# Kernel tuning notes

Measured on AMD Instinct MI355X. Metric: run time of the kernel, lower is better.

The kernel has to match this reference:

```python
import jax, jax.numpy as jnp
import numpy as np

HEADS = 8
DIM = 512
DH = DIM // HEADS          # 64
M = DIM // 2               # 256 landmarks
PINV_ITERS = 6
KER = 33                   # residual depthwise conv kernel size
EPS_LN = 1e-5


def setup_inputs() -> dict:
    key = jax.random.key(0)
    ks = jax.random.split(key, 5)
    b, n, d = 4, 8192, DIM
    inner = HEADS * DH
    x = jax.random.normal(ks[0], (b, n, d), jnp.float32)
    gamma = jnp.ones((d,), jnp.float32)
    beta = jnp.zeros((d,), jnp.float32)
    w_qkv = jax.random.normal(ks[1], (d, inner * 3), jnp.float32) * (d ** -0.5)
    res_kernel = jax.random.normal(ks[2], (HEADS, 1, KER, 1), jnp.float32) * 0.1  # depthwise (groups=heads)
    w_out = jax.random.normal(ks[3], (inner, d), jnp.float32) * (inner ** -0.5)
    b_out = jnp.zeros((d,), jnp.float32)
    return dict(x=x, gamma=gamma, beta=beta, w_qkv=w_qkv,
                res_kernel=res_kernel, w_out=w_out, b_out=b_out)


def _moore_penrose_pinv(x, iters=PINV_ITERS):
    # iterative Moore-Penrose pseudo-inverse (Razavi et al.), matches lucidrains impl
    I = jnp.eye(x.shape[-1], dtype=x.dtype)
    denom = jnp.max(jnp.sum(jnp.abs(x), axis=-1)) * jnp.max(jnp.sum(jnp.abs(x), axis=-2))
    z = jnp.swapaxes(x, -1, -2) / denom
    for _ in range(iters):
        xz = x @ z
        z = 0.25 * z @ (13.0 * I - xz @ (15.0 * I - xz @ (7.0 * I - xz)))
    return z


def _forward(x, gamma, beta, w_qkv, res_kernel, w_out, b_out):
    b, n, d = x.shape
    # pre-norm (LayerNorm)
    mu = jnp.mean(x, axis=-1, keepdims=True)
    var = jnp.var(x, axis=-1, keepdims=True)
    normed = (x - mu) / jnp.sqrt(var + EPS_LN) * gamma + beta
    # left-pad so sequence divisible by num_landmarks (static, 0 here)
    pad = (-n) % M
    xp = jnp.pad(normed, ((0, 0), (pad, 0), (0, 0)))
    N = n + pad
    qkv = xp @ w_qkv                                    # [b,N,3*h*dh]
    q, k, v = jnp.split(qkv, 3, axis=-1)
    to_heads = lambda t: t.reshape(b, N, HEADS, DH).transpose(0, 2, 1, 3)  # [b,h,N,dh]
    q = to_heads(q) * (DH ** -0.5)
    k = to_heads(k)
    v = to_heads(v)
    l = N // M
    q_l = q.reshape(b, HEADS, M, l, DH).mean(axis=3)    # [b,h,m,dh] landmarks
    k_l = k.reshape(b, HEADS, M, l, DH).mean(axis=3)
    attn1 = jax.nn.softmax(jnp.einsum('bhnd,bhmd->bhnm', q, k_l), axis=-1)   # [b,h,N,m]
    attn2 = jax.nn.softmax(jnp.einsum('bhmd,bhld->bhml', q_l, k_l), axis=-1) # [b,h,m,m]
    attn3 = jax.nn.softmax(jnp.einsum('bhmd,bhnd->bhmn', q_l, k), axis=-1)   # [b,h,m,N]
    out = attn1 @ (_moore_penrose_pinv(attn2) @ (attn3 @ v))                 # [b,h,N,dh]
    # depthwise conv residual over v (channels = heads)
    conv = jax.lax.conv_general_dilated(
        v, res_kernel, window_strides=(1, 1),
        padding=((KER // 2, KER // 2), (0, 0)),
        feature_group_count=HEADS,
        dimension_numbers=('NCHW', 'OIHW', 'NCHW'))
    out = out + conv
    out = out.transpose(0, 2, 1, 3).reshape(b, N, HEADS * DH)
    out = out @ w_out + b_out                           # to_out (dropout = identity at eval)
    out = out[:, -n:]                                   # drop left padding
    return x + out                                      # TransLayer residual


def reference(x, gamma, beta, w_qkv, res_kernel, w_out, b_out):
    return _forward(x, gamma, beta, w_qkv, res_kernel, w_out, b_out)
```

## Files before the change

### kernel.cpp

```cpp
#include <hip/hip_runtime.h>
#include <hip/hip_bf16.h>

#define B_ 4
#define N_ 8192
#define D_ 512
#define H_ 8
#define DH_ 64
#define M_ 256
#define LCH 32
#define KER_ 33
#define NSPLIT 16
#define CS (N_/NSPLIT)

typedef __hip_bfloat16 bf16;
typedef __attribute__((ext_vector_type(8))) short short8;
typedef __attribute__((ext_vector_type(4))) float f32x4;

__device__ __forceinline__ float bf2f(bf16 h){ return __bfloat162float(h); }
__device__ __forceinline__ bf16 f2bf(float f){ return __float2bfloat16(f); }
__device__ __forceinline__ f32x4 mfma16(short8 a, short8 b, f32x4 c){
  return __builtin_amdgcn_mfma_f32_16x16x32_bf16(a, b, c, 0, 0, 0);
}

__global__ __launch_bounds__(256) void k_layernorm(const float* __restrict__ x,
    const float* __restrict__ gamma, const float* __restrict__ beta,
    bf16* __restrict__ xn){
  int row = blockIdx.x;
  const float* xr = x + (size_t)row * D_;
  bf16* o = xn + (size_t)row * D_;
  int t = threadIdx.x;
  float v0 = xr[t], v1 = xr[t+256];
  float s = v0+v1, ss = v0*v0 + v1*v1;
  __shared__ float sh[8];
  for (int off=32; off; off>>=1){ s += __shfl_xor(s,off); ss += __shfl_xor(ss,off); }
  int lane = t&63, wid = t>>6;
  if (lane==0){ sh[wid] = s; sh[wid+4] = ss; }
  __syncthreads();
  float S  = sh[0]+sh[1]+sh[2]+sh[3];
  float SS = sh[4]+sh[5]+sh[6]+sh[7];
  float mu = S*(1.f/D_);
  float var = SS*(1.f/D_) - mu*mu;
  float rs = rsqrtf(var + 1e-5f);
  o[t]     = f2bf((v0-mu)*rs*gamma[t]     + beta[t]);
  o[t+256] = f2bf((v1-mu)*rs*gamma[t+256] + beta[t+256]);
}

__global__ __launch_bounds__(256) void k_wt(const float* __restrict__ W, bf16* __restrict__ WT,
    int R, int C){
  int c0 = blockIdx.x*64, r0 = blockIdx.y*64;
  __shared__ float tile[64][65];
  int t = threadIdx.x;
  for (int i=t;i<4096;i+=256){ int r=i>>6, c=i&63; tile[r][c] = W[(size_t)(r0+r)*C + c0+c]; }
  __syncthreads();
  for (int i=t;i<512;i+=256){
    int c=i>>3, rg=i&7;
    short8 o;
    #pragma unroll
    for (int j=0;j<8;j++) ((bf16*)&o)[j] = f2bf(tile[rg*8+j][c]);
    *(short8*)&WT[(size_t)(c0+c)*R + r0 + rg*8] = o;
  }
}

__global__ __launch_bounds__(256, 2) void k_mm_qkv4(const bf16* __restrict__ A, const bf16* __restrict__ WT,
    bf16* __restrict__ qbuf, bf16* __restrict__ kbuf, bf16* __restrict__ vbuf,
    bf16* __restrict__ qlb, bf16* __restrict__ klb){
  __shared__ __align__(16) bf16 smem[3*128*72];
  bf16 (*As)[72]  = (bf16(*)[72])smem;
  bf16 (*Bs0)[72] = (bf16(*)[72])(smem + 128*72);
  bf16 (*Bs1)[72] = (bf16(*)[72])(smem + 2*128*72);
  bf16 (*ebuf)[136] = (bf16(*)[136])smem;
  int t = threadIdx.x;
  int w = t>>6, lane = t&63, qd = lane>>4, n = lane&15;
  int wm = w>>1, wn = w&1;
  int r0 = blockIdx.y*128, c0 = blockIdx.x*256;
  f32x4 acc[2][4][4];
  #pragma unroll
  for (int cb=0;cb<2;cb++)
    #pragma unroll
    for (int i=0;i<4;i++)
      #pragma unroll
      for (int j=0;j<4;j++) acc[cb][i][j] = (f32x4){0.f,0.f,0.f,0.f};
  int srow = t>>3, skc = t&7;
  for (int k0=0; k0<512; k0+=64){
    #pragma unroll
    for (int ch=0; ch<4; ch++){
      int m = ch*32 + srow;
      *(short8*)&As[m][skc*8]  = *(const short8*)&A [(size_t)(r0+m)*512 + k0 + skc*8];
      *(short8*)&Bs0[m][skc*8] = *(const short8*)&WT[(size_t)(c0+m)*512 + k0 + skc*8];
      *(short8*)&Bs1[m][skc*8] = *(const short8*)&WT[(size_t)(c0+128+m)*512 + k0 + skc*8];
    }
    __syncthreads();
    #pragma unroll
    for (int ksub=0; ksub<2; ksub++){
      short8 af[4];
      #pragma unroll
      for (int i=0;i<4;i++) af[i] = *(const short8*)&As[wm*64+i*16+n][ksub*32+qd*8];
      #pragma unroll
      for (int cb=0; cb<2; cb++){
        bf16 (*Bsc)[72] = cb ? Bs1 : Bs0;
        short8 bfr[4];
        #pragma unroll
        for (int j=0;j<4;j++) bfr[j] = *(const short8*)&Bsc[wn*64+j*16+n][ksub*32+qd*8];
        #pragma unroll
        for (int i=0;i<4;i++)
          #pragma unroll
          for (int j=0;j<4;j++) acc[cb][i][j] = mfma16(af[i], bfr[j], acc[cb][i][j]);
      }
    }
    __syncthreads();
  }
  int part = c0 >> 9;
  bf16* dst = (part==0)? qbuf : (part==1)? kbuf : vbuf;
  float scale = (part==0)? 0.125f : 1.f;
  #pragma unroll
  for (int cb=0; cb<2; cb++){
    __syncthreads();
    #pragma unroll
    for (int i=0;i<4;i++)
      #pragma unroll
      for (int j=0;j<4;j++)
        #pragma unroll
        for (int rg=0; rg<4; rg++)
          ebuf[wm*64+i*16+qd*4+rg][wn*64+j*16+n] = f2bf(acc[cb][i][j][rg]*scale);
    __syncthreads();
    #pragma unroll
    for (int rep=0; rep<8; rep++){
      int unit = rep*256 + t;
      int row = unit >> 4, ch = unit & 15;
      int col = c0 + cb*128 + ch*8;
      int cc = col & 511, h = cc>>6, dh = cc&63;
      int r = r0 + row, b = r>>13, nn = r&8191;
      *(short8*)&dst[(((size_t)(b*H_+h))*N_ + nn)*DH_ + dh] = *(const short8*)&ebuf[row][ch*8];
    }
    if (part < 2){
      bf16* lt = (part==0) ? qlb : klb;
      #pragma unroll
      for (int rep=0; rep<2; rep++){
        int oi = rep*256 + t;
        int chunk = oi >> 7, col = oi & 127;
        float sum = 0.f;
        #pragma unroll
        for (int rr=0; rr<32; rr++) sum += bf2f(ebuf[chunk*32+rr][col]);
        int r = r0 + chunk*32;
        int b = r >> 13, m = (r & 8191) >> 5;
        int cc = (c0 + cb*128 + col) & 511;
        int h = cc >> 6, dh = cc & 63;
        lt[(((size_t)(b*H_+h))*M_ + m)*DH_ + dh] = f2bf(sum * (1.f/LCH));
      }
    }
  }
}

__global__ __launch_bounds__(256) void k_transp_v(const bf16* __restrict__ v, bf16* __restrict__ vT){
  int bh = blockIdx.y, n0 = blockIdx.x*64;
  __shared__ bf16 tile[64][72];
  const bf16* vb = v + (size_t)bh*N_*DH_;
  int t = threadIdx.x;
  for (int i=t; i<512; i+=256){
    int r = i>>3, cg = i&7;
    *(short8*)&tile[r][cg*8] = *(const short8*)&vb[(size_t)(n0+r)*DH_ + cg*8];
  }
  __syncthreads();
  bf16* ob = vT + (size_t)bh*DH_*N_;
  for (int i=t; i<512; i+=256){
    int dh = i>>3, ng = i&7;
    short8 o;
    #pragma unroll
    for (int j=0;j<8;j++) ((bf16*)&o)[j] = tile[ng*8+j][dh];
    *(short8*)&ob[(size_t)dh*N_ + n0 + ng*8] = o;
  }
}

__global__ __launch_bounds__(256) void k_attn2(const bf16* __restrict__ ql, const bf16* __restrict__ kl,
    float* __restrict__ A2, bf16* __restrict__ A2b){
  int bhm = blockIdx.x;
  int bh = bhm >> 8, m = bhm & 255;
  int t = threadIdx.x;
  __shared__ float qrow[64];
  __shared__ float sh[4];
  if (t < 64) qrow[t] = bf2f(ql[((size_t)bh*M_ + m)*DH_ + t]);
  __syncthreads();
  const bf16* krow = kl + ((size_t)bh*M_ + t)*DH_;
  float s = 0.f;
  #pragma unroll
  for (int i=0;i<64;i++) s += qrow[i]*bf2f(krow[i]);
  float mx = s;
  for (int off=32; off; off>>=1) mx = fmaxf(mx, __shfl_xor(mx, off));
  if ((t&63)==0) sh[t>>6] = mx;
  __syncthreads();
  mx = fmaxf(fmaxf(sh[0],sh[1]), fmaxf(sh[2],sh[3]));
  float e = expf(s - mx);
  float sum = e;
  for (int off=32; off; off>>=1) sum += __shfl_xor(sum, off);
  __syncthreads();
  if ((t&63)==0) sh[t>>6] = sum;
  __syncthreads();
  sum = sh[0]+sh[1]+sh[2]+sh[3];
  float r = e/sum;
  A2[((size_t)bh*M_ + m)*M_ + t] = r;
  A2b[((size_t)bh*M_ + m)*M_ + t] = f2bf(r);
}

__global__ __launch_bounds__(256) void k_pinv_init(const float* __restrict__ A2, bf16* __restrict__ Z){
  int bh = blockIdx.x;
  int t = threadIdx.x;
  const float* Ab = A2 + (size_t)bh*M_*M_;
  bf16* Zb = Z + (size_t)bh*M_*M_;
  float cs=0.f, rsm=0.f;
  for (int r=0;r<M_;r++) cs += fabsf(Ab[(size_t)r*M_ + t]);
  for (int c=0;c<M_;c++) rsm += fabsf(Ab[(size_t)t*M_ + c]);
  __shared__ float sh[4];
  float v = cs;
  for (int off=32; off; off>>=1) v = fmaxf(v, __shfl_xor(v, off));
  if ((t&63)==0) sh[t>>6] = v;
  __syncthreads();
  float maxc = fmaxf(fmaxf(sh[0],sh[1]), fmaxf(sh[2],sh[3]));
  __syncthreads();
  v = rsm;
  for (int off=32; off; off>>=1) v = fmaxf(v, __shfl_xor(v, off));
  if ((t&63)==0) sh[t>>6] = v;
  __syncthreads();
  float maxr = fmaxf(fmaxf(sh[0],sh[1]), fmaxf(sh[2],sh[3]));
  float inv = 1.f/(maxr*maxc);
  for (int r=0;r<M_;r++) Zb[(size_t)r*M_ + t] = f2bf(Ab[(size_t)t*M_ + r]*inv);
}

__global__ __launch_bounds__(256) void k_gemm_pmb(bf16* __restrict__ C, const bf16* __restrict__ A,
    const bf16* __restrict__ Bm, float bDiag, int bNeg, float cDiag, int cNeg, float cScale){
  int bh = blockIdx.y;
  int tm = blockIdx.x >> 2, tn = blockIdx.x & 3;
  const bf16* Ab = A  + (size_t)bh*65536;
  const bf16* Bb = Bm + (size_t)bh*65536;
  bf16* Cb = C + (size_t)bh*65536;
  __shared__ __align__(16) bf16 Ah[64][72];
  __shared__ __align__(16) bf16 Bh[64][72];
  int t = threadIdx.x;
  int w = t>>6, lane = t&63, qd = lane>>4, n = lane&15;
  int wm = w>>1, wn = w&1;
  int r0 = tm*64, c0 = tn*64;
  f32x4 acc[2][2];
  #pragma unroll
  for (int i=0;i<2;i++)
    #pragma unroll
    for (int j=0;j<2;j++) acc[i][j] = (f32x4){0.f,0.f,0.f,0.f};
  int srow = t>>3, skc = t&7;
  for (int k0=0; k0<256; k0+=64){
    #pragma unroll
    for (int ch=0; ch<2; ch++){
      int m = ch*32 + srow;
      *(short8*)&Ah[m][skc*8] = *(const short8*)&Ab[(size_t)(r0+m)*256 + k0 + skc*8];
      short8 vb = *(const short8*)&Bb[(size_t)(k0+m)*256 + c0 + skc*8];
      int kr = k0 + m;
      if (bNeg){
        #pragma unroll
        for (int j=0;j<8;j++){
          float x = (kr == (c0 + skc*8 + j) ? bDiag : 0.f) - bf2f(((bf16*)&vb)[j]);
          Bh[skc*8+j][m] = f2bf(x);
        }
      } else {
        #pragma unroll
        for (int j=0;j<8;j++) Bh[skc*8+j][m] = ((bf16*)&vb)[j];
      }
    }
    __syncthreads();
    #pragma unroll
    for (int ksub=0; ksub<2; ksub++){
      short8 afh[2], bfh[2];
      #pragma unroll
      for (int i=0;i<2;i++) afh[i] = *(const short8*)&Ah[wm*32+i*16+n][ksub*32+qd*8];
      #pragma unroll
      for (int j=0;j<2;j++) bfh[j] = *(const short8*)&Bh[wn*32+j*16+n][ksub*32+qd*8];
      #pragma unroll
      for (int i=0;i<2;i++)
        #pragma unroll
        for (int j=0;j<2;j++) acc[i][j] = mfma16(afh[i], bfh[j], acc[i][j]);
    }
    __syncthreads();
  }
  #pragma unroll
  for (int i=0;i<2;i++){
    #pragma unroll
    for (int j=0;j<2;j++){
      int cidx = c0 + wn*32 + j*16 + n;
      #pragma unroll
      for (int rg=0; rg<4; rg++){
        int r = r0 + wm*32 + i*16 + qd*4 + rg;
        float r_ = acc[i][j][rg];
        if (cNeg) r_ = ((r==cidx)? cDiag : 0.f) - r_;
        Cb[(size_t)r*256 + cidx] = f2bf(r_*cScale);
      }
    }
  }
}

__global__ __launch_bounds__(256) void k_gemm_pm(float* __restrict__ C, const void* __restrict__ Av,
    const void* __restrict__ Bv, float bDiag, int bNeg, float cDiag, int cNeg, float cScale,
    int aBf, int bBf){
  int bh = blockIdx.y;
  int tm = blockIdx.x >> 2, tn = blockIdx.x & 3;
  const float* Af = (const float*)Av; const bf16* A16 = (const bf16*)Av;
  const float* Bf = (const float*)Bv; const bf16* B16 = (const bf16*)Bv;
  float* Cb = C + (size_t)bh*65536;
  __shared__ __align__(16) bf16 Ah[64][72];
  __shared__ __align__(16) bf16 Al[64][72];
  __shared__ __align__(16) bf16 Bh[64][72];
  __shared__ __align__(16) bf16 Bl[64][72];
  int t = threadIdx.x;
  int w = t>>6, lane = t&63, qd = lane>>4, n = lane&15;
  int wm = w>>1, wn = w&1;
  int r0 = tm*64, c0 = tn*64;
  f32x4 acc[2][2];
  #pragma unroll
  for (int i=0;i<2;i++)
    #pragma unroll
    for (int j=0;j<2;j++) acc[i][j] = (f32x4){0.f,0.f,0.f,0.f};
  int srow = t>>3, skc = t&7;
  for (int k0=0; k0<256; k0+=64){
    #pragma unroll
    for (int ch=0; ch<2; ch++){
      int m = ch*32 + srow;
      if (aBf){
        *(short8*)&Ah[m][skc*8] = *(const short8*)&A16[(size_t)bh*65536 + (size_t)(r0+m)*256 + k0 + skc*8];
      } else {
        short8 vh, vl;
        const float* ap = &Af[(size_t)bh*65536 + (size_t)(r0+m)*256 + k0 + skc*8];
        #pragma unroll
        for (int j=0;j<8;j++){
          float x = ap[j];
          bf16 h = f2bf(x);
          ((bf16*)&vh)[j] = h;
          ((bf16*)&vl)[j] = f2bf(x - bf2f(h));
        }
        *(short8*)&Ah[m][skc*8] = vh;
        *(short8*)&Al[m][skc*8] = vl;
      }
      int kr = k0 + m;
      if (bBf){
        short8 vb = *(const short8*)&B16[(size_t)bh*65536 + (size_t)(k0+m)*256 + c0 + skc*8];
        #pragma unroll
        for (int j=0;j<8;j++) Bh[skc*8+j][m] = ((bf16*)&vb)[j];
      } else {
        const float* bp = &Bf[(size_t)bh*65536 + (size_t)(k0+m)*256 + c0 + skc*8];
        #pragma unroll
        for (int j=0;j<8;j++){
          float x = bp[j];
          if (bNeg) x = (kr == (c0 + skc*8 + j) ? bDiag : 0.f) - x;
          bf16 h = f2bf(x);
          Bh[skc*8+j][m] = h;
          Bl[skc*8+j][m] = f2bf(x - bf2f(h));
        }
      }
    }
    __syncthreads();
    #pragma unroll
    for (int ksub=0; ksub<2; ksub++){
      short8 afh[2], afl[2], bfh[2], bfl[2];
      #pragma unroll
      for (int i=0;i<2;i++){
        afh[i] = *(const short8*)&Ah[wm*32+i*16+n][ksub*32+qd*8];
        if (!aBf) afl[i] = *(const short8*)&Al[wm*32+i*16+n][ksub*32+qd*8];
      }
      #pragma unroll
      for (int j=0;j<2;j++){
        bfh[j] = *(const short8*)&Bh[wn*32+j*16+n][ksub*32+qd*8];
        if (!bBf) bfl[j] = *(const short8*)&Bl[wn*32+j*16+n][ksub*32+qd*8];
      }
      #pragma unroll
      for (int i=0;i<2;i++)
        #pragma unroll
        for (int j=0;j<2;j++){
          if (!aBf) acc[i][j] = mfma16(afl[i], bfh[j], acc[i][j]);
          if (!bBf) acc[i][j] = mfma16(afh[i], bfl[j], acc[i][j]);
          acc[i][j] = mfma16(afh[i], bfh[j], acc[i][j]);
        }
    }
    __syncthreads();
  }
  #pragma unroll
  for (int i=0;i<2;i++){
    #pragma unroll
    for (int j=0;j<2;j++){
      int cidx = c0 + wn*32 + j*16 + n;
      #pragma unroll
      for (int rg=0; rg<4; rg++){
        int r = r0 + wm*32 + i*16 + qd*4 + rg;
        float r_ = acc[i][j][rg];
        if (cNeg) r_ = ((r==cidx)? cDiag : 0.f) - r_;
        Cb[(size_t)r*256 + cidx] = r_*cScale;
      }
    }
  }
}

__global__ __launch_bounds__(256) void k_gemm_z2(bf16* __restrict__ z2t, const float* __restrict__ A,
    const bf16* __restrict__ Bm){
  int bh = blockIdx.y;
  int tm = blockIdx.x;
  const float* Ab = A  + (size_t)bh*65536;
  const bf16* Bb = Bm + (size_t)bh*M_*DH_;
  __shared__ float As[16][68];
  __shared__ float Bs[16][64];
  int t = threadIdx.x, tx = t&15, ty = t>>4;
  int r0 = tm*64;
  float acc[4][4] = {};
  for (int k0=0;k0<256;k0+=16){
    for (int i=t;i<1024;i+=256){
      int m=i>>4, kq=i&15;
      As[kq][m] = Ab[(size_t)(r0+m)*256 + k0+kq];
      int nn=i&63, k2=i>>6;
      Bs[k2][nn] = bf2f(Bb[(size_t)(k0+k2)*64 + nn]);
    }
    __syncthreads();
    #pragma unroll
    for (int kq=0;kq<16;kq++){
      float a0[4], b0[4];
      #pragma unroll
      for (int i=0;i<4;i++) a0[i] = As[kq][ty*4+i];
      #pragma unroll
      for (int j=0;j<4;j++) b0[j] = Bs[kq][tx*4+j];
      #pragma unroll
      for (int i=0;i<4;i++)
        #pragma unroll
        for (int j=0;j<4;j++) acc[i][j] += a0[i]*b0[j];
    }
    __syncthreads();
  }
  #pragma unroll
  for (int i=0;i<4;i++){
    int r = r0+ty*4+i;
    #pragma unroll
    for (int j=0;j<4;j++)
      z2t[(size_t)bh*16384 + (size_t)(tx*4+j)*256 + r] = f2bf(acc[i][j]);
  }
}

__global__ __launch_bounds__(256, 2) void k_flash_split(const bf16* __restrict__ Q,
    const bf16* __restrict__ K, const bf16* __restrict__ VT,
    float* __restrict__ OP, float* __restrict__ LP){
  int bh = blockIdx.y;
  int sp = blockIdx.x;
  int t = threadIdx.x, w = t>>6, lane = t&63, qd = lane>>4, n = lane&15;
  int r0 = w*64;
  const size_t Qoff = ((size_t)bh*M_ + r0)*DH_;
  const size_t Koff = ((size_t)bh*N_ + (size_t)sp*CS)*DH_;
  const size_t Voff = (size_t)bh*DH_*N_ + (size_t)sp*CS;
  __shared__ __align__(16) bf16 pbuf[4][4][16][72];
  short8 aq[4][2];
  #pragma unroll
  for (int rt=0; rt<4; rt++){
    aq[rt][0] = *(const short8*)&Q[Qoff + (size_t)(rt*16+n)*DH_ + qd*8];
    aq[rt][1] = *(const short8*)&Q[Qoff + (size_t)(rt*16+n)*DH_ + 32 + qd*8];
  }
  f32x4 o[4][4];
  float lrun[4][4];
  #pragma unroll
  for (int rt=0; rt<4; rt++){
    #pragma unroll
    for (int j=0;j<4;j++){ o[rt][j] = (f32x4){0.f,0.f,0.f,0.f}; lrun[rt][j] = 0.f; }
  }
  for (int tl=0; tl<CS/64; ++tl){
    const bf16* kp = K + Koff + (size_t)(tl*64)*DH_;
    short8 kb[4][2];
    #pragma unroll
    for (int cg=0; cg<4; cg++){
      kb[cg][0] = *(const short8*)&kp[(size_t)(cg*16+n)*DH_ + qd*8];
      kb[cg][1] = *(const short8*)&kp[(size_t)(cg*16+n)*DH_ + 32 + qd*8];
    }
    #pragma unroll
    for (int rt=0; rt<4; rt++){
      f32x4 s[4];
      #pragma unroll
      for (int cg=0; cg<4; cg++){
        f32x4 z = (f32x4){0.f,0.f,0.f,0.f};
        z = mfma16(aq[rt][0], kb[cg][0], z);
        z = mfma16(aq[rt][1], kb[cg][1], z);
        s[cg] = z;
      }
      #pragma unroll
      for (int rg=0; rg<4; rg++){
        float p0 = __expf(s[0][rg]), p1 = __expf(s[1][rg]);
        float p2 = __expf(s[2][rg]), p3 = __expf(s[3][rg]);
        float ts = p0+p1+p2+p3;
        ts += __shfl_xor(ts,1); ts += __shfl_xor(ts,2);
        ts += __shfl_xor(ts,4); ts += __shfl_xor(ts,8);
        lrun[rt][rg] += ts;
        pbuf[w][rt][qd*4+rg][n]    = f2bf(p0);
        pbuf[w][rt][qd*4+rg][16+n] = f2bf(p1);
        pbuf[w][rt][qd*4+rg][32+n] = f2bf(p2);
        pbuf[w][rt][qd*4+rg][48+n] = f2bf(p3);
      }
    }
    const bf16* vp = VT + Voff + tl*64 + qd*8;
    short8 vb[4][2];
    #pragma unroll
    for (int dg=0; dg<4; dg++){
      vb[dg][0] = *(const short8*)&vp[(size_t)(dg*16+n)*N_];
      vb[dg][1] = *(const short8*)&vp[(size_t)(dg*16+n)*N_ + 32];
    }
    #pragma unroll
    for (int rt=0; rt<4; rt++){
      short8 ap0 = *(const short8*)&pbuf[w][rt][n][qd*8];
      short8 ap1 = *(const short8*)&pbuf[w][rt][n][32+qd*8];
      #pragma unroll
      for (int dg=0; dg<4; dg++){
        o[rt][dg] = mfma16(ap0, vb[dg][0], o[rt][dg]);
        o[rt][dg] = mfma16(ap1, vb[dg][1], o[rt][dg]);
      }
    }
  }
  size_t base = ((size_t)sp*(B_*H_) + bh)*M_;
  #pragma unroll
  for (int rt=0; rt<4; rt++){
    #pragma unroll
    for (int rg=0; rg<4; rg++){
      int row = r0 + rt*16 + qd*4 + rg;
      if (n==0) LP[base+row] = lrun[rt][rg];
      #pragma unroll
      for (int dg=0; dg<4; dg++)
        OP[(base+row)*DH_ + dg*16 + n] = o[rt][dg][rg];
    }
  }
}

__global__ __launch_bounds__(256) void k_flash_merge(const float* __restrict__ OP,
    const float* __restrict__ LP, bf16* __restrict__ O){
  int bh = blockIdx.y;
  int r = blockIdx.x*4 + (threadIdx.x>>6);
  int dh = threadIdx.x & 63;
  float acc = 0.f, den = 0.f;
  for (int s=0; s<NSPLIT; s++){
    size_t base = ((size_t)s*(B_*H_) + bh)*M_ + r;
    den += LP[base];
    acc += OP[base*DH_ + dh];
  }
  O[((size_t)bh*M_ + r)*DH_ + dh] = f2bf(acc/den);
}

__global__ __launch_bounds__(256, 2) void k_flash_w3(const bf16* __restrict__ Q,
    const bf16* __restrict__ K, const bf16* __restrict__ VT, bf16* __restrict__ O){
  int bh = blockIdx.y;
  int t = threadIdx.x, w = t>>6, lane = t&63, qd = lane>>4, n = lane&15;
  int r0 = blockIdx.x*256 + w*64;
  const size_t Qoff = ((size_t)bh*N_ + r0)*DH_;
  const size_t Koff = (size_t)bh*M_*DH_;
  const size_t Voff = (size_t)bh*DH_*M_;
  __shared__ __align__(16) bf16 pbuf[4][4][16][72];
  short8 aq[4][2];
  #pragma unroll
  for (int rt=0; rt<4; rt++){
    aq[rt][0] = *(const short8*)&Q[Qoff + (size_t)(rt*16+n)*DH_ + qd*8];
    aq[rt][1] = *(const short8*)&Q[Qoff + (size_t)(rt*16+n)*DH_ + 32 + qd*8];
  }
  f32x4 o[4][4];
  float lrun[4][4];
  #pragma unroll
  for (int rt=0; rt<4; rt++){
    #pragma unroll
    for (int j=0;j<4;j++){ o[rt][j] = (f32x4){0.f,0.f,0.f,0.f}; lrun[rt][j] = 0.f; }
  }
  #pragma unroll
  for (int tl=0; tl<4; ++tl){
    const bf16* kp = K + Koff + (size_t)(tl*64)*DH_;
    short8 kb[4][2];
    #pragma unroll
    for (int cg=0; cg<4; cg++){
      kb[cg][0] = *(const short8*)&kp[(size_t)(cg*16+n)*DH_ + qd*8];
      kb[cg][1] = *(const short8*)&kp[(size_t)(cg*16+n)*DH_ + 32 + qd*8];
    }
    #pragma unroll
    for (int rt=0; rt<4; rt++){
      f32x4 s[4];
      #pragma unroll
      for (int cg=0; cg<4; cg++){
        f32x4 z = (f32x4){0.f,0.f,0.f,0.f};
        z = mfma16(aq[rt][0], kb[cg][0], z);
        z = mfma16(aq[rt][1], kb[cg][1], z);
        s[cg] = z;
      }
      #pragma unroll
      for (int rg=0; rg<4; rg++){
        float p0 = __expf(s[0][rg]), p1 = __expf(s[1][rg]);
        float p2 = __expf(s[2][rg]), p3 = __expf(s[3][rg]);
        float ts = p0+p1+p2+p3;
        ts += __shfl_xor(ts,1); ts += __shfl_xor(ts,2);
        ts += __shfl_xor(ts,4); ts += __shfl_xor(ts,8);
        lrun[rt][rg] += ts;
        pbuf[w][rt][qd*4+rg][n]    = f2bf(p0);
        pbuf[w][rt][qd*4+rg][16+n] = f2bf(p1);
        pbuf[w][rt][qd*4+rg][32+n] = f2bf(p2);
        pbuf[w][rt][qd*4+rg][48+n] = f2bf(p3);
      }
    }
    const bf16* vp = VT + Voff + tl*64 + qd*8;
    short8 vb[4][2];
    #pragma unroll
    for (int dg=0; dg<4; dg++){
      vb[dg][0] = *(const short8*)&vp[(size_t)(dg*16+n)*M_];
      vb[dg][1] = *(const short8*)&vp[(size_t)(dg*16+n)*M_ + 32];
    }
    #pragma unroll
    for (int rt=0; rt<4; rt++){
      short8 ap0 = *(const short8*)&pbuf[w][rt][n][qd*8];
      short8 ap1 = *(const short8*)&pbuf[w][rt][n][32+qd*8];
      #pragma unroll
      for (int dg=0; dg<4; dg++){
        o[rt][dg] = mfma16(ap0, vb[dg][0], o[rt][dg]);
        o[rt][dg] = mfma16(ap1, vb[dg][1], o[rt][dg]);
      }
    }
  }
  #pragma unroll
  for (int rt=0; rt<4; rt++){
    #pragma unroll
    for (int rg=0; rg<4; rg++){
      float inv = 1.f/lrun[rt][rg];
      size_t rowoff = ((size_t)bh*N_ + r0 + rt*16 + qd*4 + rg)*DH_;
      #pragma unroll
      for (int dg=0; dg<4; dg++)
        O[rowoff + dg*16 + n] = f2bf(o[rt][dg][rg]*inv);
    }
  }
}

#define CCH 256
__global__ __launch_bounds__(256) void k_conv_add(const bf16* __restrict__ v, const float* __restrict__ w,
    bf16* __restrict__ outh){
  int bh = blockIdx.y;
  int n0 = blockIdx.x * CCH;
  int h = bh & 7;
  __shared__ bf16 vs[CCH+32][72];
  __shared__ float wk[KER_];
  int t = threadIdx.x;
  if (t < KER_) wk[t] = w[h*KER_ + t];
  const bf16* vb = v + (size_t)bh*N_*DH_;
  for (int i=t; i<(CCH+32)*8; i+=256){
    int r = i>>3, cg = i&7;
    int nn = n0 - 16 + r;
    short8 val = {0,0,0,0,0,0,0,0};
    if (nn >= 0 && nn < N_) val = *(const short8*)&vb[(size_t)nn*DH_ + cg*8];
    *(short8*)&vs[r][cg*8] = val;
  }
  __syncthreads();
  int dhg = t & 7, rowg = t >> 3;
  bf16* ob = outh + ((size_t)bh*N_ + n0)*DH_;
  #pragma unroll
  for (int rr=0; rr<8; rr++){
    int lr = rowg*8 + rr;
    float acc[8] = {0.f,0.f,0.f,0.f,0.f,0.f,0.f,0.f};
    for (int tt=0; tt<KER_; tt++){
      short8 vv = *(const short8*)&vs[lr+tt][dhg*8];
      float wt = wk[tt];
      #pragma unroll
      for (int j=0;j<8;j++) acc[j] += wt * bf2f(((bf16*)&vv)[j]);
    }
    short8 o = *(short8*)&ob[(size_t)lr*DH_ + dhg*8];
    #pragma unroll
    for (int j=0;j<8;j++) ((bf16*)&o)[j] = f2bf(bf2f(((bf16*)&o)[j]) + acc[j]);
    *(short8*)&ob[(size_t)lr*DH_ + dhg*8] = o;
  }
}

__global__ __launch_bounds__(256) void k_mm_out2(const bf16* __restrict__ Ahd, const bf16* __restrict__ WT2,
    const float* __restrict__ bias, const float* __restrict__ xin, float* __restrict__ out){
  __shared__ __align__(16) bf16 As[128][72];
  __shared__ __align__(16) bf16 Bs[128][72];
  int t = threadIdx.x;
  int w = t>>6, lane = t&63, qd = lane>>4, n = lane&15;
  int wm = w>>1, wn = w&1;
  int r0 = blockIdx.y*128, c0 = blockIdx.x*128;
  f32x4 acc[4][4];
  #pragma unroll
  for (int i=0;i<4;i++)
    #pragma unroll
    for (int j=0;j<4;j++) acc[i][j] = (f32x4){0.f,0.f,0.f,0.f};
  int srow = t>>3, skc = t&7;
  for (int k0=0; k0<512; k0+=64){
    int h = k0 >> 6;
    #pragma unroll
    for (int ch=0; ch<4; ch++){
      int m = ch*32 + srow;
      int r = r0 + m, b = r>>13, nn = r&8191;
      *(short8*)&As[m][skc*8] = *(const short8*)&Ahd[((size_t)(b*H_+h)*N_ + nn)*DH_ + skc*8];
      *(short8*)&Bs[m][skc*8] = *(const short8*)&WT2[(size_t)(c0+m)*512 + k0 + skc*8];
    }
    __syncthreads();
    #pragma unroll
    for (int ksub=0; ksub<2; ksub++){
      short8 af[4], bfr[4];
      #pragma unroll
      for (int i=0;i<4;i++) af[i]  = *(const short8*)&As[wm*64+i*16+n][ksub*32+qd*8];
      #pragma unroll
      for (int j=0;j<4;j++) bfr[j] = *(const short8*)&Bs[wn*64+j*16+n][ksub*32+qd*8];
      #pragma unroll
      for (int i=0;i<4;i++)
        #pragma unroll
        for (int j=0;j<4;j++) acc[i][j] = mfma16(af[i], bfr[j], acc[i][j]);
    }
    __syncthreads();
  }
  #pragma unroll
  for (int i=0;i<4;i++){
    #pragma unroll
    for (int rg=0; rg<4; rg++){
      int r = r0 + wm*64 + i*16 + qd*4 + rg;
      size_t base = (size_t)r*512;
      #pragma unroll
      for (int j=0;j<4;j++){
        int c = c0 + wn*64 + j*16 + n;
        out[base + c] = acc[i][j][rg] + bias[c] + xin[base + c];
      }
    }
  }
}

extern "C" void kernel_launch(void* const* d_in, const int* in_sizes, int n_in,
                              void* d_out, int out_size, void* d_ws, size_t ws_size,
                              hipStream_t stream) {
  const float* x     = (const float*)d_in[0];
  const float* gamma = (const float*)d_in[1];
  const float* beta  = (const float*)d_in[2];
  const float* wqkv  = (const float*)d_in[3];
  const float* resk  = (const float*)d_in[4];
  const float* wout  = (const float*)d_in[5];
  const float* bout  = (const float*)d_in[6];
  float* out = (float*)d_out;

  const size_t SL = (size_t)B_*H_*N_*DH_;
  const size_t SM = (size_t)B_*H_*M_*DH_;
  const size_t SP = (size_t)B_*H_*M_*M_;

  bf16* xn  = (bf16*)d_ws;
  bf16* q   = xn + SL;
  bf16* k   = q + SL;
  bf16* v   = k + SL;
  bf16* vT  = v + SL;
  bf16* ql  = vT + SL;
  bf16* kl  = ql + SM;
  bf16* kv3 = kl + SM;
  bf16* z2T = kv3 + SM;
  float* A2 = (float*)(z2T + SM);
  bf16* WT  = (bf16*)(A2 + SP);
  bf16* WT2 = WT + (size_t)1536*512;
  float* P1 = (float*)xn;
  float* P2 = P1 + SP;
  float* P3 = P2 + SP;
  float* P4 = P3 + SP;
  float* OPp = (float*)xn;
  float* LPp = (float*)z2T;
  bf16* A2b = k;
  bf16* Zb0 = A2b + SP;
  bf16* Zb1 = Zb0 + SP;
  bf16* Pb  = Zb1 + SP;
  bf16* Tb  = Pb + SP;
  bf16* Ub  = Tb + SP;

  k_wt<<<dim3(24, 8), 256, 0, stream>>>(wqkv, WT, 512, 1536);
  k_wt<<<dim3(8, 8), 256, 0, stream>>>(wout, WT2, 512, 512);
  k_layernorm<<<B_*N_, 256, 0, stream>>>(x, gamma, beta, xn);
  k_mm_qkv4<<<dim3(6, 256), 256, 0, stream>>>(xn, WT, q, k, v, ql, kl);
  k_transp_v<<<dim3(128, 32), 256, 0, stream>>>(v, vT);

  k_flash_split<<<dim3(NSPLIT, B_*H_), 256, 0, stream>>>(ql, k, vT, OPp, LPp);
  k_flash_merge<<<dim3(M_/4, B_*H_), 256, 0, stream>>>(OPp, LPp, kv3);

  k_attn2<<<B_*H_*M_, 256, 0, stream>>>(ql, kl, A2, A2b);
  k_pinv_init<<<B_*H_, 256, 0, stream>>>(A2, Zb0);

  bf16* Zbi = Zb0; bf16* Zbo = Zb1;
  for (int it=0; it<4; ++it){
    k_gemm_pmb<<<dim3(16,32), 256, 0, stream>>>(Pb,  A2b, Zbi, 0.f,0, 0.f,0, 1.f);
    k_gemm_pmb<<<dim3(16,32), 256, 0, stream>>>(Tb,  Pb,  Pb,  7.f,1, 15.f,1, 1.f);
    k_gemm_pmb<<<dim3(16,32), 256, 0, stream>>>(Ub,  Pb,  Tb,  0.f,0, 13.f,1, 1.f);
    k_gemm_pmb<<<dim3(16,32), 256, 0, stream>>>(Zbo, Zbi, Ub,  0.f,0, 0.f,0, 0.25f);
    bf16* tt = Zbi; Zbi = Zbo; Zbo = tt;
  }
  k_gemm_pm<<<dim3(16,32), 256, 0, stream>>>(P2, A2, Zbi, 0.f,0, 0.f,0, 1.f,  0,1);
  k_gemm_pm<<<dim3(16,32), 256, 0, stream>>>(P3, P2, P2,  7.f,1, 15.f,1, 1.f, 0,0);
  k_gemm_pm<<<dim3(16,32), 256, 0, stream>>>(P4, P2, P3,  0.f,0, 13.f,1, 1.f, 0,0);
  k_gemm_pm<<<dim3(16,32), 256, 0, stream>>>(P1, Zbi, P4, 0.f,0, 0.f,0, 0.25f,1,0);
  k_gemm_pm<<<dim3(16,32), 256, 0, stream>>>(P2, A2, P1,  0.f,0, 0.f,0, 1.f,  0,0);
  k_gemm_pm<<<dim3(16,32), 256, 0, stream>>>(P3, P2, P2,  7.f,1, 15.f,1, 1.f, 0,0);
  k_gemm_pm<<<dim3(16,32), 256, 0, stream>>>(P4, P2, P3,  0.f,0, 13.f,1, 1.f, 0,0);
  k_gemm_pm<<<dim3(16,32), 256, 0, stream>>>(P2, P1, P4,  0.f,0, 0.f,0, 0.25f,0,0);

  k_gemm_z2<<<dim3(4, B_*H_), 256, 0, stream>>>(z2T, P2, kv3);
  k_flash_w3<<<dim3(N_/256, B_*H_), 256, 0, stream>>>(q, kl, z2T, xn);
  k_conv_add<<<dim3(N_/CCH, B_*H_), 256, 0, stream>>>(v, resk, xn);
  k_mm_out2<<<dim3(4, 256), 256, 0, stream>>>(xn, WT2, bout, x, out);
}
```

Baseline: 777.0 us.

## Fuse V transpose into QKV GEMM, remap blocks per XCD, rebalance pinv precision

The QKV GEMM epilogue now writes the transposed V buffer directly from shared memory, so the separate transpose kernel and its extra global read/write pass go away. Both the QKV and output GEMMs switch to a 1D grid with an XCD-aware block swizzle so that neighbouring tiles land on the same XCD for L2 reuse. The pseudo-inverse schedule moves one Newton-Schulz iteration from fp32 to bf16 (five bf16 plus one fp32 instead of four plus two), which cuts the slower fp32 GEMMs at some cost in accuracy.

```diff
diff --git a/kernel.cpp b/kernel.cpp
--- a/kernel.cpp
+++ b/kernel.cpp
@@ -63,7 +63,7 @@
 
 __global__ __launch_bounds__(256, 2) void k_mm_qkv4(const bf16* __restrict__ A, const bf16* __restrict__ WT,
     bf16* __restrict__ qbuf, bf16* __restrict__ kbuf, bf16* __restrict__ vbuf,
-    bf16* __restrict__ qlb, bf16* __restrict__ klb){
+    bf16* __restrict__ vT, bf16* __restrict__ qlb, bf16* __restrict__ klb){
   __shared__ __align__(16) bf16 smem[3*128*72];
   bf16 (*As)[72]  = (bf16(*)[72])smem;
   bf16 (*Bs0)[72] = (bf16(*)[72])(smem + 128*72);
@@ -72,7 +72,11 @@
   int t = threadIdx.x;
   int w = t>>6, lane = t&63, qd = lane>>4, n = lane&15;
   int wm = w>>1, wn = w&1;
-  int r0 = blockIdx.y*128, c0 = blockIdx.x*256;
+  int bid = blockIdx.x;
+  int xcd = bid & 7, pos = bid >> 3;
+  int tid = xcd*192 + pos;
+  int cx = tid % 6, ry = tid / 6;
+  int r0 = ry*128, c0 = cx*256;
   f32x4 acc[2][4][4];
   #pragma unroll
   for (int cb=0;cb<2;cb++)
@@ -112,6 +116,7 @@
   int part = c0 >> 9;
   bf16* dst = (part==0)? qbuf : (part==1)? kbuf : vbuf;
   float scale = (part==0)? 0.125f : 1.f;
+  int b = r0 >> 13, nn = r0 & 8191;
   #pragma unroll
   for (int cb=0; cb<2; cb++){
     __syncthreads();
@@ -129,8 +134,7 @@
       int row = unit >> 4, ch = unit & 15;
       int col = c0 + cb*128 + ch*8;
       int cc = col & 511, h = cc>>6, dh = cc&63;
-      int r = r0 + row, b = r>>13, nn = r&8191;
-      *(short8*)&dst[(((size_t)(b*H_+h))*N_ + nn)*DH_ + dh] = *(const short8*)&ebuf[row][ch*8];
+      *(short8*)&dst[(((size_t)(b*H_+h))*N_ + nn + row)*DH_ + dh] = *(const short8*)&ebuf[row][ch*8];
     }
     if (part < 2){
       bf16* lt = (part==0) ? qlb : klb;
@@ -141,33 +145,24 @@
         float sum = 0.f;
         #pragma unroll
         for (int rr=0; rr<32; rr++) sum += bf2f(ebuf[chunk*32+rr][col]);
-        int r = r0 + chunk*32;
-        int b = r >> 13, m = (r & 8191) >> 5;
+        int m = (nn >> 5) + chunk;
         int cc = (c0 + cb*128 + col) & 511;
         int h = cc >> 6, dh = cc & 63;
         lt[(((size_t)(b*H_+h))*M_ + m)*DH_ + dh] = f2bf(sum * (1.f/LCH));
       }
-    }
-  }
-}
-
-__global__ __launch_bounds__(256) void k_transp_v(const bf16* __restrict__ v, bf16* __restrict__ vT){
-  int bh = blockIdx.y, n0 = blockIdx.x*64;
-  __shared__ bf16 tile[64][72];
-  const bf16* vb = v + (size_t)bh*N_*DH_;
-  int t = threadIdx.x;
-  for (int i=t; i<512; i+=256){
-    int r = i>>3, cg = i&7;
-    *(short8*)&tile[r][cg*8] = *(const short8*)&vb[(size_t)(n0+r)*DH_ + cg*8];
-  }
-  __syncthreads();
-  bf16* ob = vT + (size_t)bh*DH_*N_;
-  for (int i=t; i<512; i+=256){
-    int dh = i>>3, ng = i&7;
-    short8 o;
-    #pragma unroll
-    for (int j=0;j<8;j++) ((bf16*)&o)[j] = tile[ng*8+j][dh];
-    *(short8*)&ob[(size_t)dh*N_ + n0 + ng*8] = o;
+    } else {
+      #pragma unroll
+      for (int rep=0; rep<8; rep++){
+        int unit = rep*256 + t;
+        int col = unit >> 4, rg = unit & 15;
+        int cc = (c0 + cb*128 + col) & 511;
+        int h = cc >> 6, dh = cc & 63;
+        short8 o;
+        #pragma unroll
+        for (int j=0;j<8;j++) ((bf16*)&o)[j] = ebuf[rg*8+j][col];
+        *(short8*)&vT[(((size_t)(b*H_+h))*DH_ + dh)*N_ + nn + rg*8] = o;
+      }
+    }
   }
 }
 
@@ -667,7 +662,11 @@
   int t = threadIdx.x;
   int w = t>>6, lane = t&63, qd = lane>>4, n = lane&15;
   int wm = w>>1, wn = w&1;
-  int r0 = blockIdx.y*128, c0 = blockIdx.x*128;
+  int bid = blockIdx.x;
+  int xcd = bid & 7, pos = bid >> 3;
+  int tid = xcd*128 + pos;
+  int cx = tid & 3, ry = tid >> 2;
+  int r0 = ry*128, c0 = cx*128;
   f32x4 acc[4][4];
   #pragma unroll
   for (int i=0;i<4;i++)
@@ -757,8 +756,7 @@
   k_wt<<<dim3(24, 8), 256, 0, stream>>>(wqkv, WT, 512, 1536);
   k_wt<<<dim3(8, 8), 256, 0, stream>>>(wout, WT2, 512, 512);
   k_layernorm<<<B_*N_, 256, 0, stream>>>(x, gamma, beta, xn);
-  k_mm_qkv4<<<dim3(6, 256), 256, 0, stream>>>(xn, WT, q, k, v, ql, kl);
-  k_transp_v<<<dim3(128, 32), 256, 0, stream>>>(v, vT);
+  k_mm_qkv4<<<1536, 256, 0, stream>>>(xn, WT, q, k, v, vT, ql, kl);
 
   k_flash_split<<<dim3(NSPLIT, B_*H_), 256, 0, stream>>>(ql, k, vT, OPp, LPp);
   k_flash_merge<<<dim3(M_/4, B_*H_), 256, 0, stream>>>(OPp, LPp, kv3);
@@ -767,7 +765,7 @@
   k_pinv_init<<<B_*H_, 256, 0, stream>>>(A2, Zb0);
 
   bf16* Zbi = Zb0; bf16* Zbo = Zb1;
-  for (int it=0; it<4; ++it){
+  for (int it=0; it<5; ++it){
     k_gemm_pmb<<<dim3(16,32), 256, 0, stream>>>(Pb,  A2b, Zbi, 0.f,0, 0.f,0, 1.f);
     k_gemm_pmb<<<dim3(16,32), 256, 0, stream>>>(Tb,  Pb,  Pb,  7.f,1, 15.f,1, 1.f);
     k_gemm_pmb<<<dim3(16,32), 256, 0, stream>>>(Ub,  Pb,  Tb,  0.f,0, 13.f,1, 1.f);
@@ -778,13 +776,9 @@
   k_gemm_pm<<<dim3(16,32), 256, 0, stream>>>(P3, P2, P2,  7.f,1, 15.f,1, 1.f, 0,0);
   k_gemm_pm<<<dim3(16,32), 256, 0, stream>>>(P4, P2, P3,  0.f,0, 13.f,1, 1.f, 0,0);
   k_gemm_pm<<<dim3(16,32), 256, 0, stream>>>(P1, Zbi, P4, 0.f,0, 0.f,0, 0.25f,1,0);
-  k_gemm_pm<<<dim3(16,32), 256, 0, stream>>>(P2, A2, P1,  0.f,0, 0.f,0, 1.f,  0,0);
-  k_gemm_pm<<<dim3(16,32), 256, 0, stream>>>(P3, P2, P2,  7.f,1, 15.f,1, 1.f, 0,0);
-  k_gemm_pm<<<dim3(16,32), 256, 0, stream>>>(P4, P2, P3,  0.f,0, 13.f,1, 1.f, 0,0);
-  k_gemm_pm<<<dim3(16,32), 256, 0, stream>>>(P2, P1, P4,  0.f,0, 0.f,0, 0.25f,0,0);
-
-  k_gemm_z2<<<dim3(4, B_*H_), 256, 0, stream>>>(z2T, P2, kv3);
+
+  k_gemm_z2<<<dim3(4, B_*H_), 256, 0, stream>>>(z2T, P1, kv3);
   k_flash_w3<<<dim3(N_/256, B_*H_), 256, 0, stream>>>(q, kl, z2T, xn);
   k_conv_add<<<dim3(N_/CCH, B_*H_), 256, 0, stream>>>(v, resk, xn);
-  k_mm_out2<<<dim3(4, 256), 256, 0, stream>>>(xn, WT2, bout, x, out);
-}
+  k_mm_out2<<<1024, 256, 0, stream>>>(xn, WT2, bout, x, out);
+}
```

Result: faster. 747.8 us (-3.8%).
